# Kernel optimization log

Measured on AMD Instinct MI355X. Metric: run time of the kernel, lower is better.

The kernel has to match this reference:

```python
import jax, jax.numpy as jnp
import numpy as np
import math

N_CELLS = 16384
INPUT_DIM = 512
HIDDEN = 512


def build_neighbors(n):
    n_bits = max(1, int(math.ceil(math.log2(n))))
    idx = np.arange(n)
    flips = [idx ^ (1 << b) for b in range(n_bits)]
    ring = [(idx + 1) % n, (idx - 1) % n]
    allnb = np.stack(flips + ring, axis=1)
    # dedupe per row; for power-of-2 n every row has exactly n_bits+1 uniques
    rows = [sorted(set(r.tolist())) for r in allnb]
    return np.asarray(rows, dtype=np.int32)


def setup_inputs() -> dict:
    key = jax.random.key(0)
    ks = jax.random.split(key, 12)
    n, d, h = N_CELLS, INPUT_DIM, HIDDEN
    amp = jax.random.uniform(ks[0], (n, h)) * 0.5 + 0.5
    phase = jax.random.normal(ks[1], (n, h)) * 0.3 + (2 * math.pi * jnp.arange(n) / n)[:, None]
    return {
        "x": jax.random.normal(ks[2], (1, d), dtype=jnp.float32),
        "pump_W": jax.random.normal(ks[3], (n, d), dtype=jnp.float32) / np.sqrt(d),
        "pump_b": jax.random.normal(ks[4], (n,), dtype=jnp.float32) * 0.01,
        "dec_W": jax.random.normal(ks[5], (d, 2 * h), dtype=jnp.float32) / np.sqrt(2 * h),
        "dec_b": jax.random.normal(ks[6], (d,), dtype=jnp.float32) * 0.01,
        "cs_re": (amp * jnp.cos(phase)).astype(jnp.float32),
        "cs_im": (amp * jnp.sin(phase)).astype(jnp.float32),
        "excited": jax.random.uniform(ks[7], (n,)) * 0.6,  # some cells above 0.5 threshold
        "phase_vel": jax.random.normal(ks[8], (n, h), dtype=jnp.float32) * 0.05,
        "cav_re": jax.random.normal(ks[9], (h,), dtype=jnp.float32) * 0.01,
        "cav_im": jax.random.normal(ks[10], (h,), dtype=jnp.float32) * 0.01,
        "neighbors": jnp.asarray(build_neighbors(n)),
    }


def reference(x, pump_W, pump_b, dec_W, dec_b, cs_re, cs_im, excited, phase_vel, cav_re, cav_im, neighbors):
    states = (cs_re + 1j * cs_im).astype(jnp.complex64)          # [n,h]
    cavity = (cav_re + 1j * cav_im).astype(jnp.complex64)        # [h]

    # pump + excited fraction update
    pump = jax.nn.sigmoid(x @ pump_W.T + pump_b)[0]              # [n]
    excited = jnp.clip(excited * 0.95 + pump * 0.05, 0.0, 1.0)

    # free phase rotation: polar(1, 0.1*phase_vel)
    states = states * jnp.exp(1j * (phase_vel * 0.1)).astype(jnp.complex64)

    # neighbor phase coupling (hypercube + ring, k=15 neighbors each)
    ang = jnp.angle(states)                                      # [n,h]
    nb_states = states[neighbors]                                # [n,k,h]
    coupling = jnp.cos(ang[:, None, :] - ang[neighbors])         # [n,k,h]
    interference = 0.1 * jnp.sum(coupling * nb_states, axis=1)   # [n,h]
    k = neighbors.shape[1]
    new_states = 0.7 * states + 0.3 * interference / k

    # lasing: population inversion threshold
    lasing = excited > 0.5                                       # [n]
    n_lasing = jnp.sum(lasing)
    maskf = lasing.astype(jnp.float32)[:, None]
    # emission uses pre-phase-lock states (torch copies lasing_cells first)
    emission = jnp.sum(new_states * maskf, axis=0) / jnp.maximum(n_lasing, 1).astype(jnp.float32)
    cavity_new = jnp.where(n_lasing > 0, 0.8 * cavity + 0.2 * emission, cavity)

    # phase-lock lasing cells to (old) cavity phase
    cavity_phase = jnp.angle(cavity)                             # old cavity
    new_ang = jnp.angle(new_states)
    locked = 0.3 * cavity_phase[None, :] + 0.7 * new_ang
    locked_states = jnp.abs(new_states) * jnp.exp(1j * locked)
    new_states = jnp.where(lasing[:, None], locked_states.astype(jnp.complex64), new_states)
    excited = jnp.where(lasing, excited * 0.9, excited * 0.98)

    # cavity feedback (updated cavity) + amplitude renorm
    new_states = new_states + 0.05 * cavity_new[None, :]
    amp = jnp.abs(new_states)
    amp = amp / (jnp.max(amp, axis=-1, keepdims=True) + 1e-8)
    final_states = (amp * jnp.exp(1j * jnp.angle(new_states))).astype(jnp.complex64)

    # decode cavity mode
    out_real = jnp.concatenate([cavity_new.real, cavity_new.imag])[None, :].astype(jnp.float32)  # [1,2h]
    pred = out_real @ dec_W.T + dec_b                            # [1, input_dim]
    tension = jnp.var(jnp.abs(final_states))
    return pred, tension
```

## Files before the change

### kernel.cpp

```cpp
#include <hip/hip_runtime.h>
#include <hip/hip_fp16.h>
#include <math.h>

#define N_CELLS 16384
#define HID 512
#define IND 512

#define ROT_BLOCKS  2048
#define PUMP_BLOCKS 4096

#define CPB 16
#define CELL_BLOCKS (N_CELLS / CPB)
#define PRED_BLOCKS 128

#define CNT_OFF   0
#define EMIS_OFF  128
#define CAV_OFF   4352
#define LAS_OFF   16384
#define VPART_OFF (LAS_OFF + N_CELLS*4)
#define ROT_OFF   (1<<20)
#define NST_OFF   (ROT_OFF + (size_t)N_CELLS*HID*4)

typedef unsigned int u32;

__device__ inline __half2 u2h(u32 u) { union { u32 u; __half2 h; } x; x.u = u; return x.h; }
__device__ inline u32 h2u(__half2 h) { union { u32 u; __half2 h; } x; x.h = h; return x.u; }
__device__ inline u32 packh2(float re, float im) { return h2u(__floats2half2_rn(re, im)); }
__device__ inline float2 unph2(u32 u) { __half2 h = u2h(u); return make_float2(__low2float(h), __high2float(h)); }

#if __has_builtin(__builtin_amdgcn_fdot2)
typedef _Float16 hv2 __attribute__((ext_vector_type(2)));
__device__ inline float dot2u(u32 a, u32 b) {
    union { u32 u; hv2 h; } x, y; x.u = a; y.u = b;
    return __builtin_amdgcn_fdot2(x.h, y.h, 0.f, false);
}
#else
__device__ inline float dot2u(u32 a, u32 b) {
    float2 af = unph2(a), bf = unph2(b);
    return fmaf(af.x, bf.x, af.y * bf.y);
}
#endif

__device__ inline void accnb(__half2& acc, u32 y, u32 q) {
    float d = dot2u(y, q);
    acc = __hfma2(__float2half2_rn(d), u2h(q), acc);
}

__device__ inline u32 fincell(u32 y, __half2 acc, int las, float& emR, float& emI) {
    float2 yf = unph2(y);
    float a  = fmaf(yf.x, yf.x, yf.y * yf.y);
    float rs = rsqrtf(a);
    float sq = a * rs;
    float2 af = make_float2(__low2float(acc), __high2float(acc));
    float nr = 0.7f * sq * yf.x + 0.002f * rs * af.x;
    float ni = 0.7f * sq * yf.y + 0.002f * rs * af.y;
    if (las) { emR += nr; emI += ni; }
    return packh2(nr, ni);
}

__device__ inline u32 rot1(float re, float im, float w) {
    float sc = rsqrtf(sqrtf(fmaf(re, re, im * im)));
    float s, c;
    __sincosf(0.1f * w, &s, &c);
    return packh2((re * c - im * s) * sc, (re * s + im * c) * sc);
}

__global__ __launch_bounds__(256) void k_front(const float* __restrict__ cr,
        const float* __restrict__ ci, const float* __restrict__ pv,
        u32* __restrict__ yt,
        const float* __restrict__ x, const float* __restrict__ pW,
        const float* __restrict__ pb, const float* __restrict__ excited,
        int* __restrict__ lasing, int* __restrict__ cnt) {
    int b = blockIdx.x, tid = threadIdx.x;
    if (b < ROT_BLOCKS) {
        __shared__ u32 tile[64 * 65];
        int cb = b >> 3, hb = b & 7;
        const float4* cr4 = (const float4*)cr;
        const float4* ci4 = (const float4*)ci;
        const float4* pv4 = (const float4*)pv;
#pragma unroll
        for (int j = 0; j < 4; ++j) {
            int idx = tid + 256 * j;
            int row = idx >> 4, c4 = idx & 15;
            size_t g = (size_t)(cb * 64 + row) * 128 + hb * 16 + c4;
            float4 a = cr4[g], bi = ci4[g], w = pv4[g];
            u32* dst = &tile[row * 65 + (c4 << 2)];
            dst[0] = rot1(a.x, bi.x, w.x);
            dst[1] = rot1(a.y, bi.y, w.y);
            dst[2] = rot1(a.z, bi.z, w.z);
            dst[3] = rot1(a.w, bi.w, w.w);
        }
        if (b == 0 && tid == 0) { cnt[0] = 0; cnt[1] = 0; }
        __syncthreads();
#pragma unroll
        for (int j = 0; j < 4; ++j) {
            int idx = tid + 256 * j;
            int chr = idx >> 4, c4 = idx & 15;
            uint4 v;
            v.x = tile[(c4 * 4 + 0) * 65 + chr];
            v.y = tile[(c4 * 4 + 1) * 65 + chr];
            v.z = tile[(c4 * 4 + 2) * 65 + chr];
            v.w = tile[(c4 * 4 + 3) * 65 + chr];
            ((uint4*)(yt + (size_t)(hb * 64 + chr) * N_CELLS + cb * 64))[c4] = v;
        }
    } else {
        int gtid = (b - ROT_BLOCKS) * 256 + tid;
        int cell = gtid >> 6, lane = gtid & 63;
        const float4* w4 = (const float4*)(pW + (size_t)cell * IND);
        const float4* x4 = (const float4*)x;
        float acc = 0.f;
#pragma unroll
        for (int q = 0; q < 2; ++q) {
            float4 a = w4[lane + 64 * q];
            float4 bx = x4[lane + 64 * q];
            acc += a.x * bx.x + a.y * bx.y + a.z * bx.z + a.w * bx.w;
        }
#pragma unroll
        for (int o = 32; o; o >>= 1) acc += __shfl_xor(acc, o, 64);
        if (lane == 0) {
            float p = 1.f / (1.f + expf(-(acc + pb[cell])));
            float e = excited[cell] * 0.95f + p * 0.05f;
            e = fminf(fmaxf(e, 0.f), 1.f);
            lasing[cell] = (e > 0.5f) ? 1 : 0;
        }
    }
}

__global__ __launch_bounds__(256) void k_coup(const u32* __restrict__ yt,
                                              const int* __restrict__ lasv,
                                              u32* __restrict__ nstT,
                                              float2* __restrict__ emisT,
                                              const float* __restrict__ cavr,
                                              const float* __restrict__ cavi,
                                              float* __restrict__ cavws,
                                              int* __restrict__ cnt) {
    __shared__ __align__(16) u32 col[N_CELLS];
    int ch = blockIdx.x, tid = threadIdx.x;
    const uint4* src = (const uint4*)(yt + (size_t)ch * N_CELLS);
    uint4* cdst = (uint4*)col;
#pragma unroll
    for (int k = 0; k < 16; ++k) cdst[tid + 256 * k] = src[tid + 256 * k];
    __syncthreads();

    float emR = 0.f, emI = 0.f;
    int nlo = 0;
    uint4* outp = (uint4*)(nstT + (size_t)ch * N_CELLS);
    const int4* l4 = (const int4*)lasv;
#pragma unroll 2
    for (int j = 0; j < 16; ++j) {
        int s = tid + 256 * j;
        int c = s << 2;
        uint4 sq = *(const uint4*)&col[c];
        __half2 z = __floats2half2_rn(0.f, 0.f);
        __half2 a0 = z, a1 = z, a2 = z, a3 = z;
#pragma unroll
        for (int bb = 2; bb < 14; ++bb) {
            uint4 q = *(const uint4*)&col[c ^ (1 << bb)];
            accnb(a0, sq.x, q.x);
            accnb(a1, sq.y, q.y);
            accnb(a2, sq.z, q.z);
            accnb(a3, sq.w, q.w);
        }
        u32 qm = col[(c - 1) & (N_CELLS - 1)];
        u32 qp = col[(c + 4) & (N_CELLS - 1)];
        accnb(a0, sq.x, sq.y); accnb(a0, sq.x, sq.z); accnb(a0, sq.x, qm);
        accnb(a1, sq.y, sq.x); accnb(a1, sq.y, sq.w); accnb(a1, sq.y, sq.z);
        accnb(a2, sq.z, sq.w); accnb(a2, sq.z, sq.x); accnb(a2, sq.z, sq.y);
        accnb(a3, sq.w, sq.z); accnb(a3, sq.w, sq.y); accnb(a3, sq.w, qp);
        int4 lv = l4[s];
        nlo += lv.x + lv.y + lv.z + lv.w;
        uint4 ov;
        ov.x = fincell(sq.x, a0, lv.x, emR, emI);
        ov.y = fincell(sq.y, a1, lv.y, emR, emI);
        ov.z = fincell(sq.z, a2, lv.z, emR, emI);
        ov.w = fincell(sq.w, a3, lv.w, emR, emI);
        outp[s] = ov;
    }
    __syncthreads();
#pragma unroll
    for (int o = 32; o; o >>= 1) {
        emR += __shfl_xor(emR, o, 64);
        emI += __shfl_xor(emI, o, 64);
        nlo += __shfl_xor(nlo, o, 64);
    }
    float* scr = (float*)col;
    int* iscr = (int*)col;
    int wid = tid >> 6, lane = tid & 63;
    if (lane == 0) { scr[wid] = emR; scr[4 + wid] = emI; iscr[8 + wid] = nlo; }
    __syncthreads();
    if (tid == 0) {
        emisT[ch] = make_float2(scr[0] + scr[1] + scr[2] + scr[3],
                                scr[4] + scr[5] + scr[6] + scr[7]);
        __threadfence();
        int old = atomicAdd(cnt, 1);
        iscr[12] = (old == HID - 1) ? 1 : 0;
    }
    __syncthreads();
    if (iscr[12]) {
        __threadfence();
        int nl = iscr[8] + iscr[9] + iscr[10] + iscr[11];
        float inv = (nl > 0) ? 0.2f / (float)nl : 0.f;
#pragma unroll
        for (int k2 = 0; k2 < 2; ++k2) {
            int i = tid + 256 * k2;
            float crv = cavr[i], civ = cavi[i];
            float2 e = emisT[i];
            cavws[i]        = (nl > 0) ? 0.8f * crv + e.x * inv : crv;
            cavws[512 + i]  = (nl > 0) ? 0.8f * civ + e.y * inv : civ;
            cavws[1024 + i] = atan2f(civ, crv);
        }
    }
}

__global__ __launch_bounds__(256) void k_finall(const u32* __restrict__ nstT,
        const int* __restrict__ lasv, const float* __restrict__ cavws,
        const float* __restrict__ dW, const float* __restrict__ db,
        float2* __restrict__ vpart, int* __restrict__ cnt2,
        float* __restrict__ out) {
    int b = blockIdx.x, t = threadIdx.x;
    int wid = t >> 6, lane = t & 63;
    if (b < CELL_BLOCKS) {
        __shared__ __align__(16) u32 tile[CPB * HID];
        __shared__ __align__(16) float scav[1536];
        __shared__ float w1[4], w2[4];
        __shared__ int slast;
        __shared__ double l1s[4], l2s[4];

        const float4* c4p = (const float4*)cavws;
#pragma unroll
        for (int k2 = 0; k2 < 2; ++k2) {
            int i = t + 256 * k2;
            if (i < 384) ((float4*)scav)[i] = c4p[i];
        }
        int c0 = b * CPB;
#pragma unroll
        for (int j = 0; j < 8; ++j) {
            int idx = t + 256 * j;
            int ch = idx >> 2, q = idx & 3;
            uint4 v = ((const uint4*)(nstT + (size_t)ch * N_CELLS + c0))[q];
#pragma unroll
            for (int e = 0; e < 4; ++e) {
                int cell = q * 4 + e;
                int sw = ch ^ (((e ^ q) & 1) << 4);
                tile[cell * HID + sw] = ((const u32*)&v)[e];
            }
        }
        __syncthreads();

        int cell = t >> 4, kk = t & 15;
        int lasc = lasv[c0 + cell];
        int swb = ((cell ^ (cell >> 2)) & 1) << 4;
        const u32* trow = &tile[cell * HID];
        float sa = 0.f, sa2 = 0.f, mx = 0.f;
#pragma unroll 8
        for (int i = 0; i < 32; ++i) {
            int ch = kk + 16 * i;
            float2 vf = unph2(trow[ch ^ swb]);
            float vx = vf.x, vy = vf.y;
            if (lasc) {
                float r = sqrtf(fmaf(vx, vx, vy * vy));
                float lk = 0.3f * scav[1024 + ch] + 0.7f * atan2f(vy, vx);
                float sn, cs;
                __sincosf(lk, &sn, &cs);
                vx = r * cs; vy = r * sn;
            }
            vx += 0.05f * scav[ch];
            vy += 0.05f * scav[512 + ch];
            float a2v = fmaf(vx, vx, vy * vy);
            float a = sqrtf(a2v);
            sa += a; sa2 += a2v; mx = fmaxf(mx, a);
        }
#pragma unroll
        for (int o = 1; o < 16; o <<= 1) {
            sa += __shfl_xor(sa, o, 64);
            sa2 += __shfl_xor(sa2, o, 64);
            mx = fmaxf(mx, __shfl_xor(mx, o, 64));
        }
        float invm = 1.f / (mx + 1e-8f);
        float s1 = sa * invm, s2 = sa2 * invm * invm;
        s1 += __shfl_xor(s1, 16, 64); s2 += __shfl_xor(s2, 16, 64);
        s1 += __shfl_xor(s1, 32, 64); s2 += __shfl_xor(s2, 32, 64);
        if (lane == 0) { w1[wid] = s1; w2[wid] = s2; }
        __syncthreads();
        if (t == 0) {
            vpart[b] = make_float2(w1[0] + w1[1] + w1[2] + w1[3],
                                   w2[0] + w2[1] + w2[2] + w2[3]);
            __threadfence();
            int old = atomicAdd(cnt2, 1);
            slast = (old == CELL_BLOCKS - 1) ? 1 : 0;
        }
        __syncthreads();
        if (slast) {
            __threadfence();
            double d1 = (double)vpart[t].x + (double)vpart[t + 256].x
                      + (double)vpart[t + 512].x + (double)vpart[t + 768].x;
            double d2 = (double)vpart[t].y + (double)vpart[t + 256].y
                      + (double)vpart[t + 512].y + (double)vpart[t + 768].y;
#pragma unroll
            for (int o = 32; o; o >>= 1) { d1 += __shfl_xor(d1, o, 64); d2 += __shfl_xor(d2, o, 64); }
            if (lane == 0) { l1s[wid] = d1; l2s[wid] = d2; }
            __syncthreads();
            if (t == 0) {
                double t1 = l1s[0] + l1s[1] + l1s[2] + l1s[3];
                double t2 = l2s[0] + l2s[1] + l2s[2] + l2s[3];
                double nn = (double)N_CELLS * (double)HID;
                double mean = t1 / nn;
                out[IND] = (float)(t2 / nn - mean * mean);
            }
        }
    } else {
        int j = (b - CELL_BLOCKS) * 4 + wid;
        const float4* w4 = (const float4*)(dW + (size_t)j * (2 * HID));
        const float4* o4 = (const float4*)cavws;
        float a2 = 0.f;
#pragma unroll
        for (int tt = 0; tt < 4; ++tt) {
            float4 a = w4[lane + 64 * tt];
            float4 bx = o4[lane + 64 * tt];
            a2 += a.x * bx.x + a.y * bx.y + a.z * bx.z + a.w * bx.w;
        }
#pragma unroll
        for (int o = 32; o; o >>= 1) a2 += __shfl_xor(a2, o, 64);
        if (lane == 0) out[j] = a2 + db[j];
    }
}

extern "C" void kernel_launch(void* const* d_in, const int* in_sizes, int n_in,
                              void* d_out, int out_size, void* d_ws, size_t ws_size,
                              hipStream_t stream) {
    const float* x       = (const float*)d_in[0];
    const float* pump_W  = (const float*)d_in[1];
    const float* pump_b  = (const float*)d_in[2];
    const float* dec_W   = (const float*)d_in[3];
    const float* dec_b   = (const float*)d_in[4];
    const float* cs_re   = (const float*)d_in[5];
    const float* cs_im   = (const float*)d_in[6];
    const float* excited = (const float*)d_in[7];
    const float* pvel    = (const float*)d_in[8];
    const float* cav_re  = (const float*)d_in[9];
    const float* cav_im  = (const float*)d_in[10];

    float* out = (float*)d_out;
    char* ws = (char*)d_ws;
    int*    cnt   = (int*)(ws + CNT_OFF);
    float2* emisT = (float2*)(ws + EMIS_OFF);
    float*  cavws = (float*)(ws + CAV_OFF);
    int*    lasv  = (int*)(ws + LAS_OFF);
    float2* vpart = (float2*)(ws + VPART_OFF);
    u32*    yt    = (u32*)(ws + ROT_OFF);
    u32*    nstT  = (u32*)(ws + NST_OFF);

    k_front<<<ROT_BLOCKS + PUMP_BLOCKS, 256, 0, stream>>>(
        cs_re, cs_im, pvel, yt, x, pump_W, pump_b, excited, lasv, cnt);
    k_coup<<<HID, 256, 0, stream>>>(yt, lasv, nstT, emisT, cav_re, cav_im, cavws, cnt);
    k_finall<<<CELL_BLOCKS + PRED_BLOCKS, 256, 0, stream>>>(
        nstT, lasv, cavws, dec_W, dec_b, vpart, cnt + 1, out);
}
```

Measured before the change: 265.2 us.

## Fuse three kernels into one persistent kernel with software grid barriers

Replaces the front, coupling and finalize kernels with one persistent kernel of 512 blocks of 512 threads. Stages are separated by atomic-counter grid barriers, and the barrier counters are cleared with a memset before launch. This removes two kernel launch boundaries and their tail effects. It relies on all 512 blocks being co-resident (64KB of LDS per block), and because each stage is spread over fewer blocks, parallelism per phase drops and barrier spin costs are added.

```diff
diff --git a/kernel.cpp b/kernel.cpp
--- a/kernel.cpp
+++ b/kernel.cpp
@@ -5,17 +5,11 @@
 #define N_CELLS 16384
 #define HID 512
 #define IND 512
-
-#define ROT_BLOCKS  2048
-#define PUMP_BLOCKS 4096
-
-#define CPB 16
-#define CELL_BLOCKS (N_CELLS / CPB)
-#define PRED_BLOCKS 128
+#define NB 512
+#define NT 512
 
 #define CNT_OFF   0
 #define EMIS_OFF  128
-#define CAV_OFF   4352
 #define LAS_OFF   16384
 #define VPART_OFF (LAS_OFF + N_CELLS*4)
 #define ROT_OFF   (1<<20)
@@ -65,197 +59,225 @@
     return packh2((re * c - im * s) * sc, (re * s + im * c) * sc);
 }
 
-__global__ __launch_bounds__(256) void k_front(const float* __restrict__ cr,
-        const float* __restrict__ ci, const float* __restrict__ pv,
-        u32* __restrict__ yt,
-        const float* __restrict__ x, const float* __restrict__ pW,
-        const float* __restrict__ pb, const float* __restrict__ excited,
-        int* __restrict__ lasing, int* __restrict__ cnt) {
-    int b = blockIdx.x, tid = threadIdx.x;
-    if (b < ROT_BLOCKS) {
-        __shared__ u32 tile[64 * 65];
-        int cb = b >> 3, hb = b & 7;
+__device__ inline float dot4(float4 a, float4 b) {
+    return a.x * b.x + a.y * b.y + a.z * b.z + a.w * b.w;
+}
+
+__device__ inline void gridbar(int* bar) {
+    __syncthreads();
+    if (threadIdx.x == 0) {
+        __threadfence();
+        atomicAdd(bar, 1);
+        for (int it = 0; it < (1 << 22); ++it) {
+            if (__hip_atomic_load(bar, __ATOMIC_ACQUIRE, __HIP_MEMORY_SCOPE_AGENT) >= NB) break;
+            __builtin_amdgcn_s_sleep(2);
+        }
+    }
+    __syncthreads();
+    __threadfence();
+}
+
+__global__ __launch_bounds__(NT, 4) void k_mega(
+        const float* __restrict__ cr, const float* __restrict__ ci,
+        const float* __restrict__ pv, const float* __restrict__ x,
+        const float* __restrict__ pW, const float* __restrict__ pb,
+        const float* __restrict__ excited,
+        const float* __restrict__ cavr, const float* __restrict__ cavi,
+        const float* __restrict__ dW, const float* __restrict__ db,
+        u32* __restrict__ yt, u32* __restrict__ nstT,
+        int* __restrict__ lasv, float2* __restrict__ emisT,
+        float2* __restrict__ vpart,
+        int* __restrict__ bars, float* __restrict__ out) {
+    __shared__ __align__(16) u32 col[N_CELLS];
+    int b = blockIdx.x, t = threadIdx.x;
+    int w = t >> 6, lane = t & 63;
+
+    {
         const float4* cr4 = (const float4*)cr;
         const float4* ci4 = (const float4*)ci;
         const float4* pv4 = (const float4*)pv;
-#pragma unroll
-        for (int j = 0; j < 4; ++j) {
-            int idx = tid + 256 * j;
-            int row = idx >> 4, c4 = idx & 15;
-            size_t g = (size_t)(cb * 64 + row) * 128 + hb * 16 + c4;
-            float4 a = cr4[g], bi = ci4[g], w = pv4[g];
-            u32* dst = &tile[row * 65 + (c4 << 2)];
-            dst[0] = rot1(a.x, bi.x, w.x);
-            dst[1] = rot1(a.y, bi.y, w.y);
-            dst[2] = rot1(a.z, bi.z, w.z);
-            dst[3] = rot1(a.w, bi.w, w.w);
-        }
-        if (b == 0 && tid == 0) { cnt[0] = 0; cnt[1] = 0; }
-        __syncthreads();
-#pragma unroll
-        for (int j = 0; j < 4; ++j) {
-            int idx = tid + 256 * j;
-            int chr = idx >> 4, c4 = idx & 15;
-            uint4 v;
-            v.x = tile[(c4 * 4 + 0) * 65 + chr];
-            v.y = tile[(c4 * 4 + 1) * 65 + chr];
-            v.z = tile[(c4 * 4 + 2) * 65 + chr];
-            v.w = tile[(c4 * 4 + 3) * 65 + chr];
-            ((uint4*)(yt + (size_t)(hb * 64 + chr) * N_CELLS + cb * 64))[c4] = v;
-        }
-    } else {
-        int gtid = (b - ROT_BLOCKS) * 256 + tid;
-        int cell = gtid >> 6, lane = gtid & 63;
-        const float4* w4 = (const float4*)(pW + (size_t)cell * IND);
+#pragma unroll 1
+        for (int tt = 0; tt < 4; ++tt) {
+            int tile_id = b * 4 + tt, cb = tile_id >> 3, hb = tile_id & 7;
+            float4 A[2], Bv[2], Wv[2];
+            int row[2], c4[2];
+#pragma unroll
+            for (int jj = 0; jj < 2; ++jj) {
+                int idx = t + NT * jj;
+                row[jj] = idx >> 4; c4[jj] = idx & 15;
+                size_t g = (size_t)(cb * 64 + row[jj]) * 128 + hb * 16 + c4[jj];
+                A[jj] = cr4[g]; Bv[jj] = ci4[g]; Wv[jj] = pv4[g];
+            }
+#pragma unroll
+            for (int jj = 0; jj < 2; ++jj) {
+                u32* dst = &col[row[jj] * 65 + (c4[jj] << 2)];
+                dst[0] = rot1(A[jj].x, Bv[jj].x, Wv[jj].x);
+                dst[1] = rot1(A[jj].y, Bv[jj].y, Wv[jj].y);
+                dst[2] = rot1(A[jj].z, Bv[jj].z, Wv[jj].z);
+                dst[3] = rot1(A[jj].w, Bv[jj].w, Wv[jj].w);
+            }
+            __syncthreads();
+#pragma unroll
+            for (int jj = 0; jj < 2; ++jj) {
+                int idx = t + NT * jj;
+                int chr = idx >> 4, q = idx & 15;
+                uint4 v;
+                v.x = col[(q * 4 + 0) * 65 + chr];
+                v.y = col[(q * 4 + 1) * 65 + chr];
+                v.z = col[(q * 4 + 2) * 65 + chr];
+                v.w = col[(q * 4 + 3) * 65 + chr];
+                ((uint4*)(yt + (size_t)(hb * 64 + chr) * N_CELLS + cb * 64))[q] = v;
+            }
+            __syncthreads();
+        }
+    }
+    {
         const float4* x4 = (const float4*)x;
-        float acc = 0.f;
-#pragma unroll
-        for (int q = 0; q < 2; ++q) {
-            float4 a = w4[lane + 64 * q];
-            float4 bx = x4[lane + 64 * q];
-            acc += a.x * bx.x + a.y * bx.y + a.z * bx.z + a.w * bx.w;
-        }
-#pragma unroll
-        for (int o = 32; o; o >>= 1) acc += __shfl_xor(acc, o, 64);
-        if (lane == 0) {
-            float p = 1.f / (1.f + expf(-(acc + pb[cell])));
-            float e = excited[cell] * 0.95f + p * 0.05f;
-            e = fminf(fmaxf(e, 0.f), 1.f);
-            lasing[cell] = (e > 0.5f) ? 1 : 0;
-        }
-    }
-}
-
-__global__ __launch_bounds__(256) void k_coup(const u32* __restrict__ yt,
-                                              const int* __restrict__ lasv,
-                                              u32* __restrict__ nstT,
-                                              float2* __restrict__ emisT,
-                                              const float* __restrict__ cavr,
-                                              const float* __restrict__ cavi,
-                                              float* __restrict__ cavws,
-                                              int* __restrict__ cnt) {
-    __shared__ __align__(16) u32 col[N_CELLS];
-    int ch = blockIdx.x, tid = threadIdx.x;
-    const uint4* src = (const uint4*)(yt + (size_t)ch * N_CELLS);
-    uint4* cdst = (uint4*)col;
-#pragma unroll
-    for (int k = 0; k < 16; ++k) cdst[tid + 256 * k] = src[tid + 256 * k];
-    __syncthreads();
-
-    float emR = 0.f, emI = 0.f;
-    int nlo = 0;
-    uint4* outp = (uint4*)(nstT + (size_t)ch * N_CELLS);
-    const int4* l4 = (const int4*)lasv;
+        float4 xa0 = x4[lane], xa1 = x4[lane + 64];
+        int cbase = b * 32 + w * 4;
+        float4 wv[4][2];
+#pragma unroll
+        for (int k = 0; k < 4; ++k) {
+            const float4* w4 = (const float4*)(pW + (size_t)(cbase + k) * IND);
+            wv[k][0] = w4[lane]; wv[k][1] = w4[lane + 64];
+        }
+#pragma unroll
+        for (int k = 0; k < 4; ++k) {
+            float acc = dot4(wv[k][0], xa0) + dot4(wv[k][1], xa1);
+#pragma unroll
+            for (int o = 32; o; o >>= 1) acc += __shfl_xor(acc, o, 64);
+            if (lane == 0) {
+                int cell = cbase + k;
+                float p = 1.f / (1.f + expf(-(acc + pb[cell])));
+                float e = excited[cell] * 0.95f + p * 0.05f;
+                e = fminf(fmaxf(e, 0.f), 1.f);
+                lasv[cell] = (e > 0.5f) ? 1 : 0;
+            }
+        }
+    }
+    gridbar(&bars[0]);
+
+    {
+        const uint4* src = (const uint4*)(yt + (size_t)b * N_CELLS);
+        uint4 st[8];
+#pragma unroll
+        for (int k = 0; k < 8; ++k) st[k] = src[t + NT * k];
+        uint4* cd = (uint4*)col;
+#pragma unroll
+        for (int k = 0; k < 8; ++k) cd[t + NT * k] = st[k];
+        __syncthreads();
+
+        float emR = 0.f, emI = 0.f;
+        int nlo = 0;
+        uint4* outp = (uint4*)(nstT + (size_t)b * N_CELLS);
+        const int4* l4 = (const int4*)lasv;
 #pragma unroll 2
-    for (int j = 0; j < 16; ++j) {
-        int s = tid + 256 * j;
-        int c = s << 2;
-        uint4 sq = *(const uint4*)&col[c];
-        __half2 z = __floats2half2_rn(0.f, 0.f);
-        __half2 a0 = z, a1 = z, a2 = z, a3 = z;
-#pragma unroll
-        for (int bb = 2; bb < 14; ++bb) {
-            uint4 q = *(const uint4*)&col[c ^ (1 << bb)];
-            accnb(a0, sq.x, q.x);
-            accnb(a1, sq.y, q.y);
-            accnb(a2, sq.z, q.z);
-            accnb(a3, sq.w, q.w);
-        }
-        u32 qm = col[(c - 1) & (N_CELLS - 1)];
-        u32 qp = col[(c + 4) & (N_CELLS - 1)];
-        accnb(a0, sq.x, sq.y); accnb(a0, sq.x, sq.z); accnb(a0, sq.x, qm);
-        accnb(a1, sq.y, sq.x); accnb(a1, sq.y, sq.w); accnb(a1, sq.y, sq.z);
-        accnb(a2, sq.z, sq.w); accnb(a2, sq.z, sq.x); accnb(a2, sq.z, sq.y);
-        accnb(a3, sq.w, sq.z); accnb(a3, sq.w, sq.y); accnb(a3, sq.w, qp);
-        int4 lv = l4[s];
-        nlo += lv.x + lv.y + lv.z + lv.w;
-        uint4 ov;
-        ov.x = fincell(sq.x, a0, lv.x, emR, emI);
-        ov.y = fincell(sq.y, a1, lv.y, emR, emI);
-        ov.z = fincell(sq.z, a2, lv.z, emR, emI);
-        ov.w = fincell(sq.w, a3, lv.w, emR, emI);
-        outp[s] = ov;
-    }
-    __syncthreads();
-#pragma unroll
-    for (int o = 32; o; o >>= 1) {
-        emR += __shfl_xor(emR, o, 64);
-        emI += __shfl_xor(emI, o, 64);
-        nlo += __shfl_xor(nlo, o, 64);
-    }
-    float* scr = (float*)col;
-    int* iscr = (int*)col;
-    int wid = tid >> 6, lane = tid & 63;
-    if (lane == 0) { scr[wid] = emR; scr[4 + wid] = emI; iscr[8 + wid] = nlo; }
-    __syncthreads();
-    if (tid == 0) {
-        emisT[ch] = make_float2(scr[0] + scr[1] + scr[2] + scr[3],
-                                scr[4] + scr[5] + scr[6] + scr[7]);
-        __threadfence();
-        int old = atomicAdd(cnt, 1);
-        iscr[12] = (old == HID - 1) ? 1 : 0;
-    }
-    __syncthreads();
-    if (iscr[12]) {
-        __threadfence();
-        int nl = iscr[8] + iscr[9] + iscr[10] + iscr[11];
+        for (int j = 0; j < 8; ++j) {
+            int s = t + NT * j;
+            int c = s << 2;
+            uint4 sq = *(const uint4*)&col[c];
+            __half2 z = __floats2half2_rn(0.f, 0.f);
+            __half2 a0 = z, a1 = z, a2 = z, a3 = z;
+#pragma unroll
+            for (int bb = 2; bb < 14; ++bb) {
+                uint4 q = *(const uint4*)&col[c ^ (1 << bb)];
+                accnb(a0, sq.x, q.x);
+                accnb(a1, sq.y, q.y);
+                accnb(a2, sq.z, q.z);
+                accnb(a3, sq.w, q.w);
+            }
+            u32 qm = col[(c - 1) & (N_CELLS - 1)];
+            u32 qp = col[(c + 4) & (N_CELLS - 1)];
+            accnb(a0, sq.x, sq.y); accnb(a0, sq.x, sq.z); accnb(a0, sq.x, qm);
+            accnb(a1, sq.y, sq.x); accnb(a1, sq.y, sq.w); accnb(a1, sq.y, sq.z);
+            accnb(a2, sq.z, sq.w); accnb(a2, sq.z, sq.x); accnb(a2, sq.z, sq.y);
+            accnb(a3, sq.w, sq.z); accnb(a3, sq.w, sq.y); accnb(a3, sq.w, qp);
+            int4 lv = l4[s];
+            nlo += lv.x + lv.y + lv.z + lv.w;
+            uint4 ov;
+            ov.x = fincell(sq.x, a0, lv.x, emR, emI);
+            ov.y = fincell(sq.y, a1, lv.y, emR, emI);
+            ov.z = fincell(sq.z, a2, lv.z, emR, emI);
+            ov.w = fincell(sq.w, a3, lv.w, emR, emI);
+            outp[s] = ov;
+        }
+        __syncthreads();
+#pragma unroll
+        for (int o = 32; o; o >>= 1) {
+            emR += __shfl_xor(emR, o, 64);
+            emI += __shfl_xor(emI, o, 64);
+            nlo += __shfl_xor(nlo, o, 64);
+        }
+        float* scr = (float*)col;
+        int* iscr = (int*)col;
+        if (lane == 0) { scr[w] = emR; scr[8 + w] = emI; iscr[16 + w] = nlo; }
+        __syncthreads();
+        if (t == 0) {
+            float sr = 0.f, si = 0.f; int sn = 0;
+#pragma unroll
+            for (int k = 0; k < 8; ++k) { sr += scr[k]; si += scr[8 + k]; sn += iscr[16 + k]; }
+            emisT[b] = make_float2(sr, si);
+            iscr[24] = sn;
+        }
+    }
+    gridbar(&bars[1]);
+
+    float* scav = (float*)&col[8192];
+    {
+        int nl = ((int*)col)[24];
         float inv = (nl > 0) ? 0.2f / (float)nl : 0.f;
-#pragma unroll
-        for (int k2 = 0; k2 < 2; ++k2) {
-            int i = tid + 256 * k2;
-            float crv = cavr[i], civ = cavi[i];
-            float2 e = emisT[i];
-            cavws[i]        = (nl > 0) ? 0.8f * crv + e.x * inv : crv;
-            cavws[512 + i]  = (nl > 0) ? 0.8f * civ + e.y * inv : civ;
-            cavws[1024 + i] = atan2f(civ, crv);
-        }
-    }
-}
-
-__global__ __launch_bounds__(256) void k_finall(const u32* __restrict__ nstT,
-        const int* __restrict__ lasv, const float* __restrict__ cavws,
-        const float* __restrict__ dW, const float* __restrict__ db,
-        float2* __restrict__ vpart, int* __restrict__ cnt2,
-        float* __restrict__ out) {
-    int b = blockIdx.x, t = threadIdx.x;
-    int wid = t >> 6, lane = t & 63;
-    if (b < CELL_BLOCKS) {
-        __shared__ __align__(16) u32 tile[CPB * HID];
-        __shared__ __align__(16) float scav[1536];
-        __shared__ float w1[4], w2[4];
-        __shared__ int slast;
-        __shared__ double l1s[4], l2s[4];
-
-        const float4* c4p = (const float4*)cavws;
-#pragma unroll
-        for (int k2 = 0; k2 < 2; ++k2) {
-            int i = t + 256 * k2;
-            if (i < 384) ((float4*)scav)[i] = c4p[i];
-        }
-        int c0 = b * CPB;
-#pragma unroll
-        for (int j = 0; j < 8; ++j) {
-            int idx = t + 256 * j;
-            int ch = idx >> 2, q = idx & 3;
-            uint4 v = ((const uint4*)(nstT + (size_t)ch * N_CELLS + c0))[q];
+        float crv = cavr[t], civ = cavi[t];
+        float2 e = emisT[t];
+        scav[t]        = (nl > 0) ? 0.8f * crv + e.x * inv : crv;
+        scav[512 + t]  = (nl > 0) ? 0.8f * civ + e.y * inv : civ;
+        scav[1024 + t] = atan2f(civ, crv);
+        __syncthreads();
+    }
+    if (t < 64) {
+        const float4* w4 = (const float4*)(dW + (size_t)b * (2 * HID));
+        const float4* o4 = (const float4*)scav;
+        float a2 = 0.f;
+#pragma unroll
+        for (int q = 0; q < 4; ++q) {
+            float4 a = w4[t + 64 * q];
+            float4 bx = o4[t + 64 * q];
+            a2 += dot4(a, bx);
+        }
+#pragma unroll
+        for (int o = 32; o; o >>= 1) a2 += __shfl_xor(a2, o, 64);
+        if (t == 0) out[b] = a2 + db[b];
+    }
+    float ts1 = 0.f, ts2 = 0.f;
+#pragma unroll 1
+    for (int tt = 0; tt < 2; ++tt) {
+        int c0 = b * 32 + tt * 16;
+        uint4 ld[4]; int chv[4], qv[4];
+#pragma unroll
+        for (int jj = 0; jj < 4; ++jj) {
+            int idx = t + NT * jj;
+            chv[jj] = idx >> 2; qv[jj] = idx & 3;
+            ld[jj] = ((const uint4*)(nstT + (size_t)chv[jj] * N_CELLS + c0))[qv[jj]];
+        }
+        __syncthreads();
+#pragma unroll
+        for (int jj = 0; jj < 4; ++jj) {
 #pragma unroll
             for (int e = 0; e < 4; ++e) {
-                int cell = q * 4 + e;
-                int sw = ch ^ (((e ^ q) & 1) << 4);
-                tile[cell * HID + sw] = ((const u32*)&v)[e];
-            }
-        }
-        __syncthreads();
-
-        int cell = t >> 4, kk = t & 15;
+                int cell = qv[jj] * 4 + e;
+                int sw = chv[jj] ^ (((e ^ qv[jj]) & 1) << 4);
+                col[cell * HID + sw] = ((const u32*)&ld[jj])[e];
+            }
+        }
+        __syncthreads();
+        int cell = t >> 5, kk = t & 31;
         int lasc = lasv[c0 + cell];
-        int swb = ((cell ^ (cell >> 2)) & 1) << 4;
-        const u32* trow = &tile[cell * HID];
+        int sb = ((cell ^ (cell >> 2)) & 1) << 4;
+        const u32* trow = &col[cell * HID];
         float sa = 0.f, sa2 = 0.f, mx = 0.f;
-#pragma unroll 8
-        for (int i = 0; i < 32; ++i) {
-            int ch = kk + 16 * i;
-            float2 vf = unph2(trow[ch ^ swb]);
+#pragma unroll 4
+        for (int i = 0; i < 16; ++i) {
+            int ch = kk + 32 * i;
+            float2 vf = unph2(trow[ch ^ sb]);
             float vx = vf.x, vy = vf.y;
             if (lasc) {
                 float r = sqrtf(fmaf(vx, vx, vy * vy));
@@ -271,57 +293,55 @@
             sa += a; sa2 += a2v; mx = fmaxf(mx, a);
         }
 #pragma unroll
-        for (int o = 1; o < 16; o <<= 1) {
+        for (int o = 1; o <= 16; o <<= 1) {
             sa += __shfl_xor(sa, o, 64);
             sa2 += __shfl_xor(sa2, o, 64);
             mx = fmaxf(mx, __shfl_xor(mx, o, 64));
         }
         float invm = 1.f / (mx + 1e-8f);
         float s1 = sa * invm, s2 = sa2 * invm * invm;
-        s1 += __shfl_xor(s1, 16, 64); s2 += __shfl_xor(s2, 16, 64);
-        s1 += __shfl_xor(s1, 32, 64); s2 += __shfl_xor(s2, 32, 64);
-        if (lane == 0) { w1[wid] = s1; w2[wid] = s2; }
+        s1 += __shfl_xor(s1, 32, 64);
+        s2 += __shfl_xor(s2, 32, 64);
+        ts1 += s1; ts2 += s2;
+    }
+    __syncthreads();
+    {
+        float* scr = (float*)col;
+        if (lane == 0) { scr[w] = ts1; scr[8 + w] = ts2; }
         __syncthreads();
         if (t == 0) {
-            vpart[b] = make_float2(w1[0] + w1[1] + w1[2] + w1[3],
-                                   w2[0] + w2[1] + w2[2] + w2[3]);
+            float s1 = 0.f, s2 = 0.f;
+#pragma unroll
+            for (int k = 0; k < 8; ++k) { s1 += scr[k]; s2 += scr[8 + k]; }
+            vpart[b] = make_float2(s1, s2);
+        }
+    }
+    {
+        int* iflag = (int*)&col[64];
+        if (t == 0) {
             __threadfence();
-            int old = atomicAdd(cnt2, 1);
-            slast = (old == CELL_BLOCKS - 1) ? 1 : 0;
-        }
-        __syncthreads();
-        if (slast) {
+            int old = atomicAdd(&bars[2], 1);
+            *iflag = (old == NB - 1) ? 1 : 0;
+        }
+        __syncthreads();
+        if (*iflag) {
             __threadfence();
-            double d1 = (double)vpart[t].x + (double)vpart[t + 256].x
-                      + (double)vpart[t + 512].x + (double)vpart[t + 768].x;
-            double d2 = (double)vpart[t].y + (double)vpart[t + 256].y
-                      + (double)vpart[t + 512].y + (double)vpart[t + 768].y;
+            double d1 = (double)vpart[t].x;
+            double d2 = (double)vpart[t].y;
 #pragma unroll
             for (int o = 32; o; o >>= 1) { d1 += __shfl_xor(d1, o, 64); d2 += __shfl_xor(d2, o, 64); }
-            if (lane == 0) { l1s[wid] = d1; l2s[wid] = d2; }
+            double* dscr = (double*)col;
+            if (lane == 0) { dscr[w] = d1; dscr[8 + w] = d2; }
             __syncthreads();
             if (t == 0) {
-                double t1 = l1s[0] + l1s[1] + l1s[2] + l1s[3];
-                double t2 = l2s[0] + l2s[1] + l2s[2] + l2s[3];
+                double t1 = 0.0, t2 = 0.0;
+#pragma unroll
+                for (int k = 0; k < 8; ++k) { t1 += dscr[k]; t2 += dscr[8 + k]; }
                 double nn = (double)N_CELLS * (double)HID;
                 double mean = t1 / nn;
                 out[IND] = (float)(t2 / nn - mean * mean);
             }
         }
-    } else {
-        int j = (b - CELL_BLOCKS) * 4 + wid;
-        const float4* w4 = (const float4*)(dW + (size_t)j * (2 * HID));
-        const float4* o4 = (const float4*)cavws;
-        float a2 = 0.f;
-#pragma unroll
-        for (int tt = 0; tt < 4; ++tt) {
-            float4 a = w4[lane + 64 * tt];
-            float4 bx = o4[lane + 64 * tt];
-            a2 += a.x * bx.x + a.y * bx.y + a.z * bx.z + a.w * bx.w;
-        }
-#pragma unroll
-        for (int o = 32; o; o >>= 1) a2 += __shfl_xor(a2, o, 64);
-        if (lane == 0) out[j] = a2 + db[j];
     }
 }
 
@@ -342,17 +362,15 @@
 
     float* out = (float*)d_out;
     char* ws = (char*)d_ws;
-    int*    cnt   = (int*)(ws + CNT_OFF);
+    int*    bars  = (int*)(ws + CNT_OFF);
     float2* emisT = (float2*)(ws + EMIS_OFF);
-    float*  cavws = (float*)(ws + CAV_OFF);
     int*    lasv  = (int*)(ws + LAS_OFF);
     float2* vpart = (float2*)(ws + VPART_OFF);
     u32*    yt    = (u32*)(ws + ROT_OFF);
     u32*    nstT  = (u32*)(ws + NST_OFF);
 
-    k_front<<<ROT_BLOCKS + PUMP_BLOCKS, 256, 0, stream>>>(
-        cs_re, cs_im, pvel, yt, x, pump_W, pump_b, excited, lasv, cnt);
-    k_coup<<<HID, 256, 0, stream>>>(yt, lasv, nstT, emisT, cav_re, cav_im, cavws, cnt);
-    k_finall<<<CELL_BLOCKS + PRED_BLOCKS, 256, 0, stream>>>(
-        nstT, lasv, cavws, dec_W, dec_b, vpart, cnt + 1, out);
-}
+    hipMemsetAsync(ws + CNT_OFF, 0, 16, stream);
+    k_mega<<<NB, NT, 0, stream>>>(
+        cs_re, cs_im, pvel, x, pump_W, pump_b, excited, cav_re, cav_im,
+        dec_W, dec_b, yt, nstT, lasv, emisT, vpart, bars, out);
+}
```

Result: slower. 466.0 us (+75.7%).
